# Performance work log

Hardware: AMD Instinct MI355X
Metric: run time of the kernel (lower is better)

## Reference

```python
import jax, jax.numpy as jnp
import numpy as np

B, S, D = 512, 512, 256
N_TARGETS, N_HEADS, COND_DIM = 8, 4, 64
Q = N_TARGETS * N_HEADS
NEG_INF = -1e9


def _alibi_slopes(n_heads):
    return jnp.array([2.0 ** (-8.0 * (h + 1) / n_heads) for h in range(n_heads)], dtype=jnp.float32)


def setup_inputs() -> dict:
    key = jax.random.key(0)
    ks = jax.random.split(key, 9)
    keys = jax.random.normal(ks[0], (B, S, D), dtype=jnp.float32)
    # variable-length histories: real games at positions 0..n_real-1 (oldest first)
    lengths = jax.random.randint(ks[1], (B, 1), 1, S + 1)
    mask = jnp.arange(S)[None, :] < lengths  # [B, S] bool
    context = jax.random.normal(ks[2], (B, COND_DIM), dtype=jnp.float32)
    queries = 0.02 * jax.random.normal(ks[3], (N_TARGETS, N_HEADS, D), dtype=jnp.float32)
    key_w = jax.random.normal(ks[4], (D, D), dtype=jnp.float32) / np.sqrt(D)
    value_w = jax.random.normal(ks[5], (D, D), dtype=jnp.float32) / np.sqrt(D)
    log_temperature = 0.1 * jax.random.normal(ks[6], (N_TARGETS,), dtype=jnp.float32)
    # cond_proj is zero-initialised in the original; use small random for a non-trivial path
    cond_w = 0.01 * jax.random.normal(ks[7], (Q * D, COND_DIM), dtype=jnp.float32)
    cond_b = 0.01 * jax.random.normal(ks[8], (Q * D,), dtype=jnp.float32)
    return {"keys": keys, "mask": mask, "context": context, "queries": queries,
            "key_w": key_w, "value_w": value_w, "log_temperature": log_temperature,
            "cond_w": cond_w, "cond_b": cond_b}


def reference(keys, mask, context, queries, key_w, value_w, log_temperature, cond_w, cond_b):
    scale = D ** (-0.5)
    k = jnp.einsum('bsd,ed->bse', keys, key_w)    # key_proj (no bias)
    v = jnp.einsum('bsd,ed->bse', keys, value_w)  # value_proj (no bias)
    q_flat = queries.reshape(Q, D)
    delta = (context @ cond_w.T + cond_b).reshape(-1, Q, D)  # [B, Q, D]
    q_per_row = q_flat[None] + delta
    attn = jnp.einsum('bqd,bsd->bqs', q_per_row, k) * scale  # [B, Q, S]
    # per-target learned temperature, repeat_interleave over heads
    inv_t = jnp.repeat(jnp.exp(-log_temperature), N_HEADS).reshape(1, Q, 1)
    attn = attn * inv_t
    # ALiBi time-decay bias
    n_real = mask.sum(axis=-1, keepdims=True)                 # [B, 1]
    positions = jnp.arange(S)
    games_ago = jnp.clip(n_real - 1 - positions[None, :], 0).astype(jnp.float32)  # [B, S]
    slopes = jnp.tile(_alibi_slopes(N_HEADS), N_TARGETS).reshape(1, Q, 1)
    attn = attn - slopes * games_ago[:, None, :]
    attn = jnp.where(mask[:, None, :], attn, NEG_INF)
    attn = jax.nn.softmax(attn, axis=-1)
    out = jnp.einsum('bqs,bsd->bqd', attn, v)                 # [B, Q, D]
    return out.reshape(-1, N_TARGETS, N_HEADS * D)


if __name__ == "__main__":
    out = reference(**setup_inputs())
    print(out.shape)
```

## Files before the change

kernel.cpp:

```cpp
#include <hip/hip_runtime.h>

typedef short bf16x8_t __attribute__((ext_vector_type(8)));
typedef float f32x4_t  __attribute__((ext_vector_type(4)));

#define MFMA16(a,b,c) __builtin_amdgcn_mfma_f32_16x16x32_bf16(a,b,c,0,0,0)

__device__ __forceinline__ unsigned short f2b(float x){
  unsigned u = __float_as_uint(x);
  u += 0x7fffu + ((u >> 16) & 1u);
  return (unsigned short)(u >> 16);
}

__device__ __forceinline__ void bar_lgkm(){
  asm volatile("s_waitcnt lgkmcnt(0)" ::: "memory");
  __builtin_amdgcn_s_barrier();
  __builtin_amdgcn_sched_barrier(0);
}

__global__ void setup_k(const float* __restrict__ kw, const float* __restrict__ vw,
                        const int* __restrict__ mask,
                        unsigned short* __restrict__ wktb, unsigned short* __restrict__ wvb,
                        int* __restrict__ nreal){
  int bid = blockIdx.x, tid = threadIdx.x;
  if (bid < 256){
    int i = bid * 256 + tid;
    int d = i >> 8, e = i & 255;
    wktb[i] = f2b(kw[e * 256 + d]);
    wvb[i]  = f2b(vw[i]);
  } else {
    int b = (bid - 256) * 4 + (tid >> 6), l = tid & 63;
    int s_ = 0;
    #pragma unroll
    for (int j = 0; j < 8; ++j) s_ += mask[(size_t)b * 512 + j * 64 + l];
    #pragma unroll
    for (int k = 1; k < 64; k <<= 1) s_ += __shfl_xor(s_, k);
    if (l == 0) nreal[b] = s_ < 1 ? 1 : (s_ > 512 ? 512 : s_);
  }
}

__global__ __launch_bounds__(256) void calc_qs(
    const float* __restrict__ context, const float* __restrict__ queries,
    const float* __restrict__ logt, const float* __restrict__ condw,
    const float* __restrict__ condb, unsigned short* __restrict__ qs){
  __shared__ float ctx_l[8 * 64];
  int tid = threadIdx.x;
  int q   = blockIdx.x & 31;
  int b0  = (blockIdx.x >> 5) * 8;
  int qd  = q * 256 + tid;
  float4 cw[16];
  #pragma unroll
  for (int j = 0; j < 16; ++j) cw[j] = *(const float4*)(condw + (size_t)qd * 64 + 4 * j);
  float qbias = queries[qd] + condb[qd];
  float sc = 0.0625f * __expf(-logt[q >> 2]);
  ctx_l[tid]       = context[(size_t)b0 * 64 + tid];
  ctx_l[tid + 256] = context[(size_t)b0 * 64 + tid + 256];
  __syncthreads();
  #pragma unroll
  for (int b = 0; b < 8; ++b){
    const float4* cl = (const float4*)(ctx_l + b * 64);
    float acc = 0.f;
    #pragma unroll
    for (int j = 0; j < 16; ++j){
      float4 cv = cl[j]; float4 w4 = cw[j];
      acc += cv.x * w4.x + cv.y * w4.y + cv.z * w4.z + cv.w * w4.w;
    }
    qs[((size_t)(b0 + b) * 32 + q) * 256 + tid] = f2b((qbias + acc) * sc);
  }
}

__global__ __launch_bounds__(256) void calc_qkp(
    const unsigned short* __restrict__ qs, const unsigned short* __restrict__ wkt,
    unsigned short* __restrict__ qkp){
  __shared__ unsigned short at[64 * 256];
  int tid = threadIdx.x, w = tid >> 6, l = tid & 63, h = l >> 4, c = l & 15;
  size_t r0 = (size_t)blockIdx.x * 64;
  #pragma unroll
  for (int j = 0; j < 8; ++j){
    int f = j * 256 + tid;
    int row = f >> 5, col = (f & 31) * 8;
    bf16x8_t v = *(const bf16x8_t*)(qs + (r0 + row) * 256 + col);
    *(bf16x8_t*)&at[row * 256 + (col ^ ((row & 7) << 3))] = v;
  }
  __syncthreads();
  f32x4_t zero4 = {0.f, 0.f, 0.f, 0.f};
  f32x4_t acc[4][4];
  #pragma unroll
  for (int mt = 0; mt < 4; ++mt)
    #pragma unroll
    for (int nt = 0; nt < 4; ++nt) acc[mt][nt] = zero4;
  #pragma unroll
  for (int kk = 0; kk < 8; ++kk){
    bf16x8_t A[4];
    #pragma unroll
    for (int mt = 0; mt < 4; ++mt){
      int row = c + 16 * mt;
      A[mt] = *(const bf16x8_t*)&at[row * 256 + ((kk * 32 + 8 * h) ^ ((row & 7) << 3))];
    }
    #pragma unroll
    for (int nt = 0; nt < 4; ++nt){
      int d = 64 * w + 16 * nt + c;
      bf16x8_t Bv = *(const bf16x8_t*)(wkt + (size_t)d * 256 + kk * 32 + 8 * h);
      #pragma unroll
      for (int mt = 0; mt < 4; ++mt) acc[mt][nt] = MFMA16(A[mt], Bv, acc[mt][nt]);
    }
  }
  #pragma unroll
  for (int mt = 0; mt < 4; ++mt)
    #pragma unroll
    for (int nt = 0; nt < 4; ++nt)
      #pragma unroll
      for (int i = 0; i < 4; ++i){
        size_t row = r0 + 16 * mt + 4 * h + i;
        int d = 64 * w + 16 * nt + c;
        qkp[row * 256 + d] = f2b(acc[mt][nt][i]);
      }
}

__global__ __launch_bounds__(256, 2) void attn_part(
    const float* __restrict__ keys, const int* __restrict__ nreal,
    const unsigned short* __restrict__ qkp, const unsigned short* __restrict__ wvb,
    float* __restrict__ out){
  __shared__ unsigned short K[64 * 256];
  __shared__ unsigned short vT[256 * 64];
  __shared__ unsigned short Pl[32 * 64];
  __shared__ float denl[32];

  int b = (blockIdx.x & 7) * 64 + (blockIdx.x >> 3);
  int n_real = nreal[b];

  int tid = threadIdx.x, w = tid >> 6, l = tid & 63, h = l >> 4, c = l & 15;
  int qg = w & 1, rp = w >> 1;
  if (tid < 32) denl[tid] = 0.f;

  bf16x8_t bIe, bIo;
  #pragma unroll
  for (int j = 0; j < 8; ++j){
    bIe[j] = (h == (c >> 3)     && j == (c & 7)) ? (short)0x3F80 : (short)0;
    bIo[j] = (h == 2 + (c >> 3) && j == (c & 7)) ? (short)0x3F80 : (short)0;
  }

  const float* kptr = keys + ((size_t)b * 512 + w) * 256 + 4 * l;
  float4 R[16];
  #pragma unroll
  for (int j = 0; j < 16; ++j) R[j] = *(const float4*)(kptr + j * 1024);

  bf16x8_t qf[8];
  #pragma unroll
  for (int kk = 0; kk < 8; ++kk)
    qf[kk] = *(const bf16x8_t*)(qkp + ((size_t)b * 32 + 16 * qg + c) * 256 + kk * 32 + 8 * h);

  float slope0 = exp2f(-2.0f * (float)((c & 3) + 1));

  f32x4_t zero4 = {0.f, 0.f, 0.f, 0.f};
  f32x4_t ao[2][4];
  #pragma unroll
  for (int q2 = 0; q2 < 2; ++q2)
    #pragma unroll
    for (int nt = 0; nt < 4; ++nt) ao[q2][nt] = zero4;

  int tend = (n_real + 63) >> 6;

  for (int it = 0; it < tend; ++it){
    int s0 = it * 64;
    const float* knext = kptr + (size_t)(it + 1) * (64 * 256);
    #pragma unroll
    for (int j = 0; j < 16; ++j){
      int row = 4 * j + w;
      int d4 = 4 * l;
      float4 kv = R[j];
      if (it + 1 < tend) R[j] = *(const float4*)(knext + j * 1024);
      uint2 p;
      p.x = (unsigned)f2b(kv.x) | ((unsigned)f2b(kv.y) << 16);
      p.y = (unsigned)f2b(kv.z) | ((unsigned)f2b(kv.w) << 16);
      *(uint2*)&K[row * 256 + (d4 ^ ((row & 7) << 3))] = p;
    }
    bar_lgkm();

    f32x4_t as_[2];
    as_[0] = zero4; as_[1] = zero4;
    #pragma unroll
    for (int kk = 0; kk < 8; ++kk){
      int colk = kk * 32 + 8 * h;
      {
        int r0_ = 16 * (2 * rp) + c, r1_ = 16 * (2 * rp + 1) + c;
        bf16x8_t A0 = *(const bf16x8_t*)&K[r0_ * 256 + (colk ^ ((r0_ & 7) << 3))];
        bf16x8_t A1 = *(const bf16x8_t*)&K[r1_ * 256 + (colk ^ ((r1_ & 7) << 3))];
        as_[0] = MFMA16(A0, qf[kk], as_[0]);
        as_[1] = MFMA16(A1, qf[kk], as_[1]);
      }
      if ((kk >> 1) == w){
        int ntb = (kk & 1) << 1;
        int e0 = 64 * w + 16 * ntb + c;
        int e1 = e0 + 16;
        #pragma unroll
        for (int g = 0; g < 4; ++g){
          int rg_ = 16 * g + c;
          bf16x8_t Ag = *(const bf16x8_t*)&K[rg_ * 256 + (colk ^ ((rg_ & 7) << 3))];
          f32x4_t tE = MFMA16(Ag, bIe, zero4);
          f32x4_t tO = MFMA16(Ag, bIo, zero4);
          int t0 = 16 * g + 4 * h;
          uint2 p;
          p.x = (unsigned)f2b(tE[0]) | ((unsigned)f2b(tE[1]) << 16);
          p.y = (unsigned)f2b(tE[2]) | ((unsigned)f2b(tE[3]) << 16);
          *(uint2*)&vT[e0 * 64 + (t0 ^ ((e0 & 7) << 3))] = p;
          p.x = (unsigned)f2b(tO[0]) | ((unsigned)f2b(tO[1]) << 16);
          p.y = (unsigned)f2b(tO[2]) | ((unsigned)f2b(tO[3]) << 16);
          *(uint2*)&vT[e1 * 64 + (t0 ^ ((e1 & 7) << 3))] = p;
        }
      }
    }

    {
      float qs_ = 0.f;
      int q = 16 * qg + c;
      #pragma unroll
      for (int g2 = 0; g2 < 2; ++g2){
        int gr = 2 * rp + g2;
        float e_[4];
        #pragma unroll
        for (int i = 0; i < 4; ++i){
          int s = s0 + 16 * gr + 4 * h + i;
          float ga = (float)(n_real - 1 - s);
          bool valid = (s < n_real);
          float v = valid ? __expf(as_[g2][i] - slope0 * ga) : 0.f;
          e_[i] = v; qs_ += v;
        }
        int t0 = 16 * gr + 4 * h;
        uint2 p;
        p.x = (unsigned)f2b(e_[0]) | ((unsigned)f2b(e_[1]) << 16);
        p.y = (unsigned)f2b(e_[2]) | ((unsigned)f2b(e_[3]) << 16);
        *(uint2*)&Pl[q * 64 + (t0 ^ ((q & 7) << 3))] = p;
      }
      float r = qs_ + __shfl_xor(qs_, 16); r += __shfl_xor(r, 32);
      if (l < 16) atomicAdd(&denl[q], r);
    }
    bar_lgkm();

    #pragma unroll
    for (int ts = 0; ts < 2; ++ts){
      int t0 = 32 * ts + 8 * h;
      bf16x8_t Ap0 = *(const bf16x8_t*)&Pl[c * 64 + (t0 ^ ((c & 7) << 3))];
      bf16x8_t Ap1 = *(const bf16x8_t*)&Pl[(16 + c) * 64 + (t0 ^ (((16 + c) & 7) << 3))];
      #pragma unroll
      for (int nt = 0; nt < 4; ++nt){
        int e = 64 * w + 16 * nt + c;
        bf16x8_t Bv = *(const bf16x8_t*)&vT[e * 64 + (t0 ^ ((e & 7) << 3))];
        ao[0][nt] = MFMA16(Ap0, Bv, ao[0][nt]);
        ao[1][nt] = MFMA16(Ap1, Bv, ao[1][nt]);
      }
    }
  }

  {
    unsigned short* at = K;
    #pragma unroll
    for (int q2 = 0; q2 < 2; ++q2)
      #pragma unroll
      for (int i = 0; i < 4; ++i){
        int q = 16 * q2 + 4 * h + i;
        float invd = 1.f / denl[q];
        #pragma unroll
        for (int nt = 0; nt < 4; ++nt){
          int e = 64 * w + 16 * nt + c;
          at[q * 256 + (e ^ ((q & 7) << 3))] = f2b(ao[q2][nt][i] * invd);
        }
      }
    __syncthreads();

    f32x4_t zero4b = {0.f, 0.f, 0.f, 0.f};
    f32x4_t a2[2][4];
    #pragma unroll
    for (int m = 0; m < 2; ++m)
      #pragma unroll
      for (int nt = 0; nt < 4; ++nt) a2[m][nt] = zero4b;
    #pragma unroll
    for (int kk = 0; kk < 8; ++kk){
      bf16x8_t A[2];
      #pragma unroll
      for (int m = 0; m < 2; ++m){
        int row = c + 16 * m;
        A[m] = *(const bf16x8_t*)&at[row * 256 + ((kk * 32 + 8 * h) ^ ((row & 7) << 3))];
      }
      #pragma unroll
      for (int nt = 0; nt < 4; ++nt){
        int ep = 64 * w + 16 * nt + c;
        bf16x8_t Bv = *(const bf16x8_t*)(wvb + (size_t)ep * 256 + kk * 32 + 8 * h);
        #pragma unroll
        for (int m = 0; m < 2; ++m) a2[m][nt] = MFMA16(A[m], Bv, a2[m][nt]);
      }
    }
    #pragma unroll
    for (int m = 0; m < 2; ++m)
      #pragma unroll
      for (int nt = 0; nt < 4; ++nt)
        #pragma unroll
        for (int i = 0; i < 4; ++i){
          int row = 16 * m + 4 * h + i;
          int ep = 64 * w + 16 * nt + c;
          out[((size_t)b * 32 + row) * 256 + ep] = a2[m][nt][i];
        }
  }
}

extern "C" void kernel_launch(void* const* d_in, const int* in_sizes, int n_in,
                              void* d_out, int out_size, void* d_ws, size_t ws_size,
                              hipStream_t stream){
  const float* keys    = (const float*)d_in[0];
  const int*   mask    = (const int*)d_in[1];
  const float* context = (const float*)d_in[2];
  const float* queries = (const float*)d_in[3];
  const float* key_w   = (const float*)d_in[4];
  const float* value_w = (const float*)d_in[5];
  const float* logt    = (const float*)d_in[6];
  const float* cond_w  = (const float*)d_in[7];
  const float* cond_b  = (const float*)d_in[8];
  float* out = (float*)d_out;

  unsigned short* wkt = (unsigned short*)d_ws;
  unsigned short* wvb = wkt + 65536;
  unsigned short* qs  = wvb + 65536;
  unsigned short* qkp = qs + (size_t)16384 * 256;
  int*   nreal = (int*)(qkp + (size_t)16384 * 256);

  hipLaunchKernelGGL(setup_k,  dim3(384), dim3(256), 0, stream, key_w, value_w, mask, wkt, wvb, nreal);
  hipLaunchKernelGGL(calc_qs,  dim3(2048), dim3(256), 0, stream, context, queries, logt, cond_w, cond_b, qs);
  hipLaunchKernelGGL(calc_qkp, dim3(256), dim3(256), 0, stream, qs, wkt, qkp);
  hipLaunchKernelGGL(attn_part, dim3(512), dim3(256), 0, stream, keys, nreal, qkp, wvb, out);
}
```

Before: 86.35 us.

## Fuse setup kernels and compute query-key projection inside attention kernel

Merges setup_k and calc_qs into one launch and removes the calc_qkp kernel. Each attention block now computes its 32x256 q·Wk projection with MFMA, staging the result through the vT shared buffer. This cuts two kernel launches and the global round-trip of the qkp intermediate. In exchange the attention kernel does extra MFMA work and shared-memory traffic at its start, before the main loop.

```diff
diff --git a/kernel.cpp b/kernel.cpp
--- a/kernel.cpp
+++ b/kernel.cpp
@@ -17,18 +17,47 @@
   __builtin_amdgcn_sched_barrier(0);
 }
 
-__global__ void setup_k(const float* __restrict__ kw, const float* __restrict__ vw,
-                        const int* __restrict__ mask,
-                        unsigned short* __restrict__ wktb, unsigned short* __restrict__ wvb,
-                        int* __restrict__ nreal){
+__global__ __launch_bounds__(256) void setup_qs(
+    const float* __restrict__ context, const float* __restrict__ queries,
+    const float* __restrict__ logt, const float* __restrict__ condw,
+    const float* __restrict__ condb,
+    const float* __restrict__ kw, const float* __restrict__ vw,
+    const int* __restrict__ mask,
+    unsigned short* __restrict__ qs,
+    unsigned short* __restrict__ wktb, unsigned short* __restrict__ wvb,
+    int* __restrict__ nreal){
   int bid = blockIdx.x, tid = threadIdx.x;
-  if (bid < 256){
-    int i = bid * 256 + tid;
+  if (bid < 2048){
+    __shared__ float ctx_l[8 * 64];
+    int q   = bid & 31;
+    int b0  = (bid >> 5) * 8;
+    int qd  = q * 256 + tid;
+    float4 cw[16];
+    #pragma unroll
+    for (int j = 0; j < 16; ++j) cw[j] = *(const float4*)(condw + (size_t)qd * 64 + 4 * j);
+    float qbias = queries[qd] + condb[qd];
+    float sc = 0.0625f * __expf(-logt[q >> 2]);
+    ctx_l[tid]       = context[(size_t)b0 * 64 + tid];
+    ctx_l[tid + 256] = context[(size_t)b0 * 64 + tid + 256];
+    __syncthreads();
+    #pragma unroll
+    for (int b = 0; b < 8; ++b){
+      const float4* cl = (const float4*)(ctx_l + b * 64);
+      float acc = 0.f;
+      #pragma unroll
+      for (int j = 0; j < 16; ++j){
+        float4 cv = cl[j]; float4 w4 = cw[j];
+        acc += cv.x * w4.x + cv.y * w4.y + cv.z * w4.z + cv.w * w4.w;
+      }
+      qs[((size_t)(b0 + b) * 32 + q) * 256 + tid] = f2b((qbias + acc) * sc);
+    }
+  } else if (bid < 2304){
+    int i = (bid - 2048) * 256 + tid;
     int d = i >> 8, e = i & 255;
     wktb[i] = f2b(kw[e * 256 + d]);
     wvb[i]  = f2b(vw[i]);
   } else {
-    int b = (bid - 256) * 4 + (tid >> 6), l = tid & 63;
+    int b = (bid - 2304) * 4 + (tid >> 6), l = tid & 63;
     int s_ = 0;
     #pragma unroll
     for (int j = 0; j < 8; ++j) s_ += mask[(size_t)b * 512 + j * 64 + l];
@@ -38,88 +67,10 @@
   }
 }
 
-__global__ __launch_bounds__(256) void calc_qs(
-    const float* __restrict__ context, const float* __restrict__ queries,
-    const float* __restrict__ logt, const float* __restrict__ condw,
-    const float* __restrict__ condb, unsigned short* __restrict__ qs){
-  __shared__ float ctx_l[8 * 64];
-  int tid = threadIdx.x;
-  int q   = blockIdx.x & 31;
-  int b0  = (blockIdx.x >> 5) * 8;
-  int qd  = q * 256 + tid;
-  float4 cw[16];
-  #pragma unroll
-  for (int j = 0; j < 16; ++j) cw[j] = *(const float4*)(condw + (size_t)qd * 64 + 4 * j);
-  float qbias = queries[qd] + condb[qd];
-  float sc = 0.0625f * __expf(-logt[q >> 2]);
-  ctx_l[tid]       = context[(size_t)b0 * 64 + tid];
-  ctx_l[tid + 256] = context[(size_t)b0 * 64 + tid + 256];
-  __syncthreads();
-  #pragma unroll
-  for (int b = 0; b < 8; ++b){
-    const float4* cl = (const float4*)(ctx_l + b * 64);
-    float acc = 0.f;
-    #pragma unroll
-    for (int j = 0; j < 16; ++j){
-      float4 cv = cl[j]; float4 w4 = cw[j];
-      acc += cv.x * w4.x + cv.y * w4.y + cv.z * w4.z + cv.w * w4.w;
-    }
-    qs[((size_t)(b0 + b) * 32 + q) * 256 + tid] = f2b((qbias + acc) * sc);
-  }
-}
-
-__global__ __launch_bounds__(256) void calc_qkp(
-    const unsigned short* __restrict__ qs, const unsigned short* __restrict__ wkt,
-    unsigned short* __restrict__ qkp){
-  __shared__ unsigned short at[64 * 256];
-  int tid = threadIdx.x, w = tid >> 6, l = tid & 63, h = l >> 4, c = l & 15;
-  size_t r0 = (size_t)blockIdx.x * 64;
-  #pragma unroll
-  for (int j = 0; j < 8; ++j){
-    int f = j * 256 + tid;
-    int row = f >> 5, col = (f & 31) * 8;
-    bf16x8_t v = *(const bf16x8_t*)(qs + (r0 + row) * 256 + col);
-    *(bf16x8_t*)&at[row * 256 + (col ^ ((row & 7) << 3))] = v;
-  }
-  __syncthreads();
-  f32x4_t zero4 = {0.f, 0.f, 0.f, 0.f};
-  f32x4_t acc[4][4];
-  #pragma unroll
-  for (int mt = 0; mt < 4; ++mt)
-    #pragma unroll
-    for (int nt = 0; nt < 4; ++nt) acc[mt][nt] = zero4;
-  #pragma unroll
-  for (int kk = 0; kk < 8; ++kk){
-    bf16x8_t A[4];
-    #pragma unroll
-    for (int mt = 0; mt < 4; ++mt){
-      int row = c + 16 * mt;
-      A[mt] = *(const bf16x8_t*)&at[row * 256 + ((kk * 32 + 8 * h) ^ ((row & 7) << 3))];
-    }
-    #pragma unroll
-    for (int nt = 0; nt < 4; ++nt){
-      int d = 64 * w + 16 * nt + c;
-      bf16x8_t Bv = *(const bf16x8_t*)(wkt + (size_t)d * 256 + kk * 32 + 8 * h);
-      #pragma unroll
-      for (int mt = 0; mt < 4; ++mt) acc[mt][nt] = MFMA16(A[mt], Bv, acc[mt][nt]);
-    }
-  }
-  #pragma unroll
-  for (int mt = 0; mt < 4; ++mt)
-    #pragma unroll
-    for (int nt = 0; nt < 4; ++nt)
-      #pragma unroll
-      for (int i = 0; i < 4; ++i){
-        size_t row = r0 + 16 * mt + 4 * h + i;
-        int d = 64 * w + 16 * nt + c;
-        qkp[row * 256 + d] = f2b(acc[mt][nt][i]);
-      }
-}
-
 __global__ __launch_bounds__(256, 2) void attn_part(
     const float* __restrict__ keys, const int* __restrict__ nreal,
-    const unsigned short* __restrict__ qkp, const unsigned short* __restrict__ wvb,
-    float* __restrict__ out){
+    const unsigned short* __restrict__ qs, const unsigned short* __restrict__ wkt,
+    const unsigned short* __restrict__ wvb, float* __restrict__ out){
   __shared__ unsigned short K[64 * 256];
   __shared__ unsigned short vT[256 * 64];
   __shared__ unsigned short Pl[32 * 64];
@@ -131,6 +82,8 @@
   int tid = threadIdx.x, w = tid >> 6, l = tid & 63, h = l >> 4, c = l & 15;
   int qg = w & 1, rp = w >> 1;
   if (tid < 32) denl[tid] = 0.f;
+
+  f32x4_t zero4 = {0.f, 0.f, 0.f, 0.f};
 
   bf16x8_t bIe, bIo;
   #pragma unroll
@@ -145,13 +98,44 @@
   for (int j = 0; j < 16; ++j) R[j] = *(const float4*)(kptr + j * 1024);
 
   bf16x8_t qf[8];
-  #pragma unroll
-  for (int kk = 0; kk < 8; ++kk)
-    qf[kk] = *(const bf16x8_t*)(qkp + ((size_t)b * 32 + 16 * qg + c) * 256 + kk * 32 + 8 * h);
+  {
+    unsigned short* qtmp = vT;
+    f32x4_t qa[4][2];
+    #pragma unroll
+    for (int mt = 0; mt < 4; ++mt){ qa[mt][0] = zero4; qa[mt][1] = zero4; }
+    #pragma unroll
+    for (int kk = 0; kk < 8; ++kk){
+      int colk = kk * 32 + 8 * h;
+      bf16x8_t B0 = *(const bf16x8_t*)(qs + ((size_t)b * 32 + c) * 256 + colk);
+      bf16x8_t B1 = *(const bf16x8_t*)(qs + ((size_t)b * 32 + 16 + c) * 256 + colk);
+      #pragma unroll
+      for (int mt = 0; mt < 4; ++mt){
+        int d = 64 * w + 16 * mt + c;
+        bf16x8_t Av = *(const bf16x8_t*)(wkt + (size_t)d * 256 + colk);
+        qa[mt][0] = MFMA16(Av, B0, qa[mt][0]);
+        qa[mt][1] = MFMA16(Av, B1, qa[mt][1]);
+      }
+    }
+    #pragma unroll
+    for (int mt = 0; mt < 4; ++mt)
+      #pragma unroll
+      for (int qt2 = 0; qt2 < 2; ++qt2)
+        #pragma unroll
+        for (int i = 0; i < 4; ++i){
+          int q = 16 * qt2 + c;
+          int d = 64 * w + 16 * mt + 4 * h + i;
+          qtmp[q * 256 + (d ^ ((q & 7) << 3))] = f2b(qa[mt][qt2][i]);
+        }
+    bar_lgkm();
+    #pragma unroll
+    for (int kk = 0; kk < 8; ++kk){
+      int q = 16 * qg + c;
+      qf[kk] = *(const bf16x8_t*)&qtmp[q * 256 + ((kk * 32 + 8 * h) ^ ((q & 7) << 3))];
+    }
+  }
 
   float slope0 = exp2f(-2.0f * (float)((c & 3) + 1));
 
-  f32x4_t zero4 = {0.f, 0.f, 0.f, 0.f};
   f32x4_t ao[2][4];
   #pragma unroll
   for (int q2 = 0; q2 < 2; ++q2)
@@ -267,12 +251,11 @@
       }
     __syncthreads();
 
-    f32x4_t zero4b = {0.f, 0.f, 0.f, 0.f};
     f32x4_t a2[2][4];
     #pragma unroll
     for (int m = 0; m < 2; ++m)
       #pragma unroll
-      for (int nt = 0; nt < 4; ++nt) a2[m][nt] = zero4b;
+      for (int nt = 0; nt < 4; ++nt) a2[m][nt] = zero4;
     #pragma unroll
     for (int kk = 0; kk < 8; ++kk){
       bf16x8_t A[2];
@@ -319,11 +302,10 @@
   unsigned short* wkt = (unsigned short*)d_ws;
   unsigned short* wvb = wkt + 65536;
   unsigned short* qs  = wvb + 65536;
-  unsigned short* qkp = qs + (size_t)16384 * 256;
-  int*   nreal = (int*)(qkp + (size_t)16384 * 256);
-
-  hipLaunchKernelGGL(setup_k,  dim3(384), dim3(256), 0, stream, key_w, value_w, mask, wkt, wvb, nreal);
-  hipLaunchKernelGGL(calc_qs,  dim3(2048), dim3(256), 0, stream, context, queries, logt, cond_w, cond_b, qs);
-  hipLaunchKernelGGL(calc_qkp, dim3(256), dim3(256), 0, stream, qs, wkt, qkp);
-  hipLaunchKernelGGL(attn_part, dim3(512), dim3(256), 0, stream, keys, nreal, qkp, wvb, out);
-}
+  int*   nreal = (int*)(qs + (size_t)16384 * 256);
+
+  hipLaunchKernelGGL(setup_qs, dim3(2432), dim3(256), 0, stream,
+                     context, queries, logt, cond_w, cond_b, key_w, value_w, mask,
+                     qs, wkt, wvb, nreal);
+  hipLaunchKernelGGL(attn_part, dim3(512), dim3(256), 0, stream, keys, nreal, qs, wkt, wvb, out);
+}
```

New measurement: 81.55 us (median of 3 runs). 5.6% less time.
